# Optimization experiments

Measured on AMD Instinct MI355X. Metric: run time of the kernel, lower is better.

## Reference

```python
import jax, jax.numpy as jnp
import numpy as np

B, D, H, E, TOP_K = 16384, 256, 1024, 8, 2


def setup_inputs() -> dict:
    key = jax.random.key(0)
    ks = jax.random.split(key, 12)
    s = 0.02
    return {
        "t": jax.random.uniform(ks[0], (B,), dtype=jnp.float32),
        "x": jax.random.normal(ks[1], (B, D), dtype=jnp.float32),
        # router: Linear(D+1,H) -> SiLU -> Linear(H,E)
        "Rw1": jax.random.normal(ks[2], (D + 1, H), dtype=jnp.float32) * s,
        "Rb1": jnp.zeros((H,), dtype=jnp.float32),
        "Rw2": jax.random.normal(ks[3], (H, E), dtype=jnp.float32) * s,
        "Rb2": jnp.zeros((E,), dtype=jnp.float32),
        # stacked expert MLPs: (D+1)->H->H->D for each of E experts
        "Ew1": jax.random.normal(ks[4], (E, D + 1, H), dtype=jnp.float32) * s,
        "Eb1": jnp.zeros((E, H), dtype=jnp.float32),
        "Ew2": jax.random.normal(ks[5], (E, H, H), dtype=jnp.float32) * s,
        "Eb2": jnp.zeros((E, H), dtype=jnp.float32),
        "Ew3": jax.random.normal(ks[6], (E, H, D), dtype=jnp.float32) * s,
        "Eb3": jnp.zeros((E, D), dtype=jnp.float32),
    }


def reference(t, x, Rw1, Rb1, Rw2, Rb2, Ew1, Eb1, Ew2, Eb2, Ew3, Eb3):
    t_vec = t.reshape(-1, 1)                      # (B,1)
    xt = jnp.concatenate([x, t_vec], axis=-1)     # (B,D+1)

    # router logits
    h = jax.nn.silu(xt @ Rw1 + Rb1)
    logits = h @ Rw2 + Rb2                        # (B,E)

    # top-k sparse gating (top_k < num_experts)
    topk_vals, topk_idx = jax.lax.top_k(logits, TOP_K)
    mask = jnp.zeros_like(logits).at[jnp.arange(logits.shape[0])[:, None], topk_idx].set(1.0)
    masked_logits = jnp.where(mask == 0, -jnp.inf, logits)
    alpha = jax.nn.softmax(masked_logits, axis=-1)  # (B,E)

    # dense all-expert MLPs (faithful to the original stack+einsum)
    h1 = jax.nn.silu(jnp.einsum('bi,eih->beh', xt, Ew1) + Eb1)   # (B,E,H)
    h2 = jax.nn.silu(jnp.einsum('beh,ehg->beg', h1, Ew2) + Eb2)  # (B,E,H)
    expert_out = jnp.einsum('beh,ehd->bed', h2, Ew3) + Eb3       # (B,E,D)

    velocity = jnp.einsum('be,bed->bd', alpha, expert_out)       # (B,D)
    return velocity
```

## Files before the change

### kernel.cpp

```cpp
#include <hip/hip_runtime.h>
#include <cstdint>
#include <cstddef>

#define NB   16384
#define DD   256
#define DIN  257
#define KP1  288
#define HH   1024
#define NE   8
#define GMAX 33792
#define GMT  264

#define CTRL_INTS 272

typedef unsigned short u16;
typedef __bf16 bf16x8 __attribute__((ext_vector_type(8)));
typedef float  f32x4  __attribute__((ext_vector_type(4)));
typedef unsigned short u16x4 __attribute__((ext_vector_type(4)));

__device__ __forceinline__ u16 f2bf(float f) {
  union { float f; unsigned u; } v; v.f = f;
  return (u16)((v.u + 0x7FFFu + ((v.u >> 16) & 1u)) >> 16);
}
__device__ __forceinline__ float bf2f(u16 h) {
  union { unsigned u; float f; } v; v.u = ((unsigned)h) << 16;
  return v.f;
}

#define GLDS16(g, l) __builtin_amdgcn_global_load_lds( \
    (const __attribute__((address_space(1))) void*)(g), \
    (__attribute__((address_space(3))) void*)(l), 16, 0, 0)

__device__ __forceinline__ int swz_u16(int row, int q) {
  return row * 32 + ((q ^ ((row >> 1) & 3)) * 8);
}

__global__ void build_xt3(const float* __restrict__ x, const float* __restrict__ t,
                          u16* __restrict__ xh, u16* __restrict__ xm, u16* __restrict__ xl) {
  long i = (long)blockIdx.x * 256 + threadIdx.x;
  int b = (int)(i / 72), qd = (int)(i % 72);
  f32x4 v;
  if (qd < 64)       v = *(const f32x4*)&x[(long)b * DD + qd * 4];
  else if (qd == 64) v = (f32x4){t[b], 0.f, 0.f, 0.f};
  else               v = (f32x4){0.f, 0.f, 0.f, 0.f};
  u16x4 h, m, l;
  #pragma unroll
  for (int j = 0; j < 4; ++j) {
    u16 hi = f2bf(v[j]);  float r1 = v[j] - bf2f(hi);
    u16 mi = f2bf(r1);    float r2 = r1 - bf2f(mi);
    h[j] = hi; m[j] = mi; l[j] = f2bf(r2);
  }
  long o = (long)b * KP1 + qd * 4;
  *(u16x4*)&xh[o] = h;  *(u16x4*)&xm[o] = m;  *(u16x4*)&xl[o] = l;
}

__global__ void transpose_w(const float* __restrict__ W, u16* __restrict__ Wh,
                            u16* __restrict__ Wm, u16* __restrict__ Wl,
                            int Kdim, int Ndim, int Kpad, long sW, long sWt) {
  __shared__ float tile[32][33];
  int e = blockIdx.z;
  int k0 = blockIdx.x * 32, n0 = blockIdx.y * 32;
  int tx = threadIdx.x, ty = threadIdx.y;
  const float* Wb = W + (long)e * sW;
  #pragma unroll
  for (int i = 0; i < 4; ++i) {
    int k = k0 + ty + i * 8;
    tile[ty + i * 8][tx] = (k < Kdim) ? Wb[(long)k * Ndim + (n0 + tx)] : 0.f;
  }
  __syncthreads();
  #pragma unroll
  for (int i = 0; i < 4; ++i) {
    int n = n0 + ty + i * 8;
    float v = tile[tx][ty + i * 8];
    long o = (long)e * sWt + (long)n * Kpad + k0 + tx;
    u16 hi = f2bf(v);
    Wh[o] = hi;
    if (Wm) {
      float r1 = v - bf2f(hi);
      u16 mi = f2bf(r1);
      Wm[o] = mi;
      Wl[o] = f2bf(r1 - bf2f(mi));
    }
  }
}

__global__ __launch_bounds__(256, 2)
void router_gemm_emul3(const u16* __restrict__ Ah, const u16* __restrict__ Am, const u16* __restrict__ Al,
                       const u16* __restrict__ Bh, const u16* __restrict__ Bm, const u16* __restrict__ Bl,
                       const float* __restrict__ bias, const float* __restrict__ Rw2,
                       float* __restrict__ pbuf) {
  __shared__ __align__(16) u16 S[6][128 * 32];
  int tid = threadIdx.x;
  int bid = blockIdx.x;
  int xcd = bid & 7, j = bid >> 3;
  int mt = (j >> 3) * 8 + xcd, nt = j & 7;
  int m0 = mt * 128, n0 = nt * 128;
  const u16* Ap[3] = {Ah, Am, Al};
  const u16* Bp[3] = {Bh, Bm, Bl};
  const u16 *ag[3][2], *bg[3][2];
  u16 *la[3][2], *lb[3][2];
  #pragma unroll
  for (int r = 0; r < 2; ++r) {
    int i = r * 256 + tid;
    int row = i >> 2;
    int qa = (i & 3) ^ ((row >> 1) & 3);
    int kq = qa * 8;
    #pragma unroll
    for (int p = 0; p < 3; ++p) {
      ag[p][r] = Ap[p] + (long)(m0 + row) * KP1 + kq;
      bg[p][r] = Bp[p] + (long)(n0 + row) * KP1 + kq;
      la[p][r] = &S[p][i * 8];
      lb[p][r] = &S[3 + p][i * 8];
    }
  }
  int lane = tid & 63, wv = tid >> 6;
  int wm = wv >> 1, wn = wv & 1;
  int q = lane >> 4, c = lane & 15;
  int offA[4], offB[4];
  #pragma unroll
  for (int t4 = 0; t4 < 4; ++t4) {
    offA[t4] = swz_u16(wm * 64 + t4 * 16 + c, q);
    offB[t4] = swz_u16(wn * 64 + t4 * 16 + c, q);
  }
  f32x4 acc[4][4];
  #pragma unroll
  for (int mi = 0; mi < 4; ++mi)
    #pragma unroll
    for (int ni = 0; ni < 4; ++ni) acc[mi][ni] = (f32x4){0.f, 0.f, 0.f, 0.f};

  for (int k0 = 0; k0 < KP1; k0 += 32) {
    __syncthreads();
    #pragma unroll
    for (int r = 0; r < 2; ++r)
      #pragma unroll
      for (int p = 0; p < 3; ++p) {
        GLDS16(ag[p][r] + k0, la[p][r]);
        GLDS16(bg[p][r] + k0, lb[p][r]);
      }
    __syncthreads();
    bf16x8 av[3][4], bv[3][4];
    #pragma unroll
    for (int mi = 0; mi < 4; ++mi)
      #pragma unroll
      for (int p = 0; p < 3; ++p) av[p][mi] = *(const bf16x8*)&S[p][offA[mi]];
    #pragma unroll
    for (int ni = 0; ni < 4; ++ni)
      #pragma unroll
      for (int p = 0; p < 3; ++p) bv[p][ni] = *(const bf16x8*)&S[3 + p][offB[ni]];
    #pragma unroll
    for (int mi = 0; mi < 4; ++mi)
      #pragma unroll
      for (int ni = 0; ni < 4; ++ni) {
        acc[mi][ni] = __builtin_amdgcn_mfma_f32_16x16x32_bf16(av[0][mi], bv[0][ni], acc[mi][ni], 0, 0, 0);
        acc[mi][ni] = __builtin_amdgcn_mfma_f32_16x16x32_bf16(av[0][mi], bv[1][ni], acc[mi][ni], 0, 0, 0);
        acc[mi][ni] = __builtin_amdgcn_mfma_f32_16x16x32_bf16(av[1][mi], bv[0][ni], acc[mi][ni], 0, 0, 0);
        acc[mi][ni] = __builtin_amdgcn_mfma_f32_16x16x32_bf16(av[0][mi], bv[2][ni], acc[mi][ni], 0, 0, 0);
        acc[mi][ni] = __builtin_amdgcn_mfma_f32_16x16x32_bf16(av[2][mi], bv[0][ni], acc[mi][ni], 0, 0, 0);
      }
  }
  float rw2f[4][8];
  #pragma unroll
  for (int ni = 0; ni < 4; ++ni) {
    const float* p = Rw2 + (long)(n0 + wn * 64 + ni * 16 + c) * NE;
    f32x4 a = *(const f32x4*)p, b2 = *(const f32x4*)(p + 4);
    #pragma unroll
    for (int j2 = 0; j2 < 4; ++j2) { rw2f[ni][j2] = a[j2]; rw2f[ni][4 + j2] = b2[j2]; }
  }
  float bi[4];
  #pragma unroll
  for (int ni = 0; ni < 4; ++ni) bi[ni] = bias[n0 + wn * 64 + ni * 16 + c];
  #pragma unroll
  for (int mi = 0; mi < 4; ++mi)
    #pragma unroll
    for (int r = 0; r < 4; ++r) {
      int token = m0 + wm * 64 + mi * 16 + q * 4 + r;
      float part[8] = {0.f, 0.f, 0.f, 0.f, 0.f, 0.f, 0.f, 0.f};
      #pragma unroll
      for (int ni = 0; ni < 4; ++ni) {
        float v = acc[mi][ni][r] + bi[ni];
        v = v / (1.f + expf(-v));
        #pragma unroll
        for (int e = 0; e < 8; ++e) part[e] += v * rw2f[ni][e];
      }
      #pragma unroll
      for (int m = 1; m < 16; m <<= 1)
        #pragma unroll
        for (int e = 0; e < 8; ++e) part[e] += __shfl_xor(part[e], m, 64);
      if (c == 0) {
        float* dst = pbuf + ((long)(nt * 2 + wn) * NB + token) * 8;
        *(f32x4*)dst       = (f32x4){part[0], part[1], part[2], part[3]};
        *(f32x4*)(dst + 4) = (f32x4){part[4], part[5], part[6], part[7]};
      }
    }
}

__global__ void reduce_topk(const float* __restrict__ pbuf, const float* __restrict__ Rb2,
                            int* __restrict__ tk_idx, float* __restrict__ tk_alpha,
                            int* __restrict__ ctrl) {
  __shared__ int lh[NE];
  int tid = threadIdx.x;
  if (tid < NE) lh[tid] = 0;
  __syncthreads();
  int token = blockIdx.x * 256 + tid;
  float v[8];
  #pragma unroll
  for (int e = 0; e < 8; ++e) v[e] = Rb2[e];
  #pragma unroll
  for (int p = 0; p < 16; ++p) {
    const float* src = pbuf + ((long)p * NB + token) * 8;
    f32x4 a = *(const f32x4*)src, b = *(const f32x4*)(src + 4);
    #pragma unroll
    for (int j = 0; j < 4; ++j) { v[j] += a[j]; v[4 + j] += b[j]; }
  }
  int i0 = 0;
  #pragma unroll
  for (int e = 1; e < NE; ++e) if (v[e] > v[i0]) i0 = e;
  int i1 = -1;
  #pragma unroll
  for (int e = 0; e < NE; ++e) { if (e == i0) continue; if (i1 < 0 || v[e] > v[i1]) i1 = e; }
  float d  = v[i1] - v[i0];
  float e1 = expf(d);
  float a0 = 1.f / (1.f + e1);
  float a1 = e1 / (1.f + e1);
  tk_idx[token * 2]     = i0;  tk_idx[token * 2 + 1]   = i1;
  tk_alpha[token * 2]   = a0;  tk_alpha[token * 2 + 1] = a1;
  atomicAdd(&lh[i0], 1);  atomicAdd(&lh[i1], 1);
  __syncthreads();
  if (tid < NE) atomicAdd(&ctrl[tid * 16], lh[tid]);
}

__global__ void compute_offsets(int* __restrict__ ctrl) {
  if (threadIdx.x == 0 && blockIdx.x == 0) {
    int total = 0;
    for (int e = 0; e < NE; ++e) {
      ctrl[256 + e] = total;
      total += (ctrl[e * 16] + 127) & ~127;
    }
    ctrl[256 + NE] = total;
  }
}

__global__ void build_rowmap(const int* __restrict__ tk_idx, int* __restrict__ ctrl,
                             int* __restrict__ grow, int* __restrict__ tok2slot) {
  __shared__ int lh[NE];
  __shared__ int gb[NE];
  int tid = threadIdx.x;
  if (tid < NE) lh[tid] = 0;
  __syncthreads();
  int token = blockIdx.x * 256 + tid;
  int e0 = tk_idx[token * 2], e1 = tk_idx[token * 2 + 1];
  int l0 = atomicAdd(&lh[e0], 1);
  int l1 = atomicAdd(&lh[e1], 1);
  __syncthreads();
  if (tid < NE) gb[tid] = atomicAdd(&ctrl[128 + tid * 16], lh[tid]);
  __syncthreads();
  int g0 = ctrl[256 + e0] + gb[e0] + l0;
  int g1 = ctrl[256 + e1] + gb[e1] + l1;
  grow[g0] = token;  grow[g1] = token;
  tok2slot[token * 2] = g0;  tok2slot[token * 2 + 1] = g1;
}

template<int NKT, int NT, bool GATHER, bool SILU, bool OUTF32>
__global__ __launch_bounds__(256, 2)
void gemm_grouped(const u16* __restrict__ A, int lda,
                  const u16* __restrict__ Wt, long wstride, int ldw,
                  const float* __restrict__ bias, int bstride,
                  u16* __restrict__ C, int ldc,
                  float* __restrict__ Out, int ldo,
                  const int* __restrict__ offp,
                  const int* __restrict__ grow,
                  int K) {
  int bid = blockIdx.x;
  int xcd = bid & 7, j = bid >> 3;
  int mt = (j / NT) * 8 + xcd, nt = j % NT;
  int m0 = mt * 128, n0 = nt * 128;
  if (m0 >= offp[NE]) return;
  int e = 0;
  while (m0 >= offp[e + 1]) ++e;
  __shared__ __align__(16) u16 As[NKT][128 * 32];
  __shared__ __align__(16) u16 Bs[NKT][128 * 32];
  int tid = threadIdx.x;
  const u16 *ag[NKT][2], *bg[NKT][2];
  u16 *la[NKT][2], *lb[NKT][2];
  #pragma unroll
  for (int s = 0; s < NKT; ++s)
    #pragma unroll
    for (int r = 0; r < 2; ++r) {
      int i = r * 256 + tid;
      int row = i >> 2;
      int qa = (i & 3) ^ ((row >> 1) & 3);
      int kq = qa * 8 + s * 32;
      long arow = m0 + row;
      if (GATHER) arow = grow[arow];
      ag[s][r] = A + arow * lda + kq;
      bg[s][r] = Wt + (long)e * wstride + (long)(n0 + row) * ldw + kq;
      la[s][r] = &As[s][i * 8];
      lb[s][r] = &Bs[s][i * 8];
    }
  int lane = tid & 63, wv = tid >> 6;
  int wm = wv >> 1, wn = wv & 1;
  int q = lane >> 4, c = lane & 15;
  int offA[4], offB[4];
  #pragma unroll
  for (int t4 = 0; t4 < 4; ++t4) {
    offA[t4] = swz_u16(wm * 64 + t4 * 16 + c, q);
    offB[t4] = swz_u16(wn * 64 + t4 * 16 + c, q);
  }
  f32x4 acc[4][4];
  #pragma unroll
  for (int mi = 0; mi < 4; ++mi)
    #pragma unroll
    for (int ni = 0; ni < 4; ++ni) acc[mi][ni] = (f32x4){0.f, 0.f, 0.f, 0.f};

  for (int k0 = 0; k0 < K; k0 += 32 * NKT) {
    __syncthreads();
    #pragma unroll
    for (int s = 0; s < NKT; ++s)
      #pragma unroll
      for (int r = 0; r < 2; ++r) {
        GLDS16(ag[s][r] + k0, la[s][r]);
        GLDS16(bg[s][r] + k0, lb[s][r]);
      }
    __syncthreads();
    #pragma unroll
    for (int s = 0; s < NKT; ++s) {
      bf16x8 av[4], bv[4];
      #pragma unroll
      for (int mi = 0; mi < 4; ++mi)
        av[mi] = *(const bf16x8*)&As[s][offA[mi]];
      #pragma unroll
      for (int ni = 0; ni < 4; ++ni)
        bv[ni] = *(const bf16x8*)&Bs[s][offB[ni]];
      #pragma unroll
      for (int mi = 0; mi < 4; ++mi)
        #pragma unroll
        for (int ni = 0; ni < 4; ++ni)
          acc[mi][ni] = __builtin_amdgcn_mfma_f32_16x16x32_bf16(av[mi], bv[ni], acc[mi][ni], 0, 0, 0);
    }
  }
  #pragma unroll
  for (int mi = 0; mi < 4; ++mi)
    #pragma unroll
    for (int r = 0; r < 4; ++r) {
      int row = wm * 64 + mi * 16 + q * 4 + r;
      #pragma unroll
      for (int ni = 0; ni < 4; ++ni) {
        int col = n0 + wn * 64 + ni * 16 + c;
        float v = acc[mi][ni][r] + bias[e * bstride + col];
        if constexpr (SILU) v = v / (1.f + __expf(-v));
        if constexpr (OUTF32) {
          Out[(long)(m0 + row) * ldo + col] = v;
        } else {
          C[(long)(m0 + row) * ldc + col] = f2bf(v);
        }
      }
    }
}

__global__ void combine_out(const float* __restrict__ eo, const int* __restrict__ tok2slot,
                            const float* __restrict__ tk_alpha, float* __restrict__ out) {
  int i = blockIdx.x * 256 + threadIdx.x;
  int token = i >> 6, c4 = (i & 63) * 4;
  long s0 = tok2slot[token * 2], s1 = tok2slot[token * 2 + 1];
  float a0 = tk_alpha[token * 2], a1 = tk_alpha[token * 2 + 1];
  f32x4 v0 = *(const f32x4*)&eo[s0 * DD + c4];
  f32x4 v1 = *(const f32x4*)&eo[s1 * DD + c4];
  f32x4 r;
  #pragma unroll
  for (int j = 0; j < 4; ++j) r[j] = a0 * v0[j] + a1 * v1[j];
  *(f32x4*)&out[(long)token * DD + c4] = r;
}

extern "C" void kernel_launch(void* const* d_in, const int* in_sizes, int n_in,
                              void* d_out, int out_size, void* d_ws, size_t ws_size,
                              hipStream_t stream) {
  const float* t   = (const float*)d_in[0];
  const float* x   = (const float*)d_in[1];
  const float* Rw1 = (const float*)d_in[2];
  const float* Rb1 = (const float*)d_in[3];
  const float* Rw2 = (const float*)d_in[4];
  const float* Rb2 = (const float*)d_in[5];
  const float* Eb1 = (const float*)d_in[7];
  const float* Ew1 = (const float*)d_in[6];
  const float* Ew2 = (const float*)d_in[8];
  const float* Eb2 = (const float*)d_in[9];
  const float* Ew3 = (const float*)d_in[10];
  const float* Eb3 = (const float*)d_in[11];
  float* out = (float*)d_out;

  char* w = (char*)d_ws;
  size_t off = 0;
  auto alloc = [&](size_t bytes) { char* p = w + off; off = (off + bytes + 255) & ~(size_t)255; return p; };
  int*   ctrl     = (int*)  alloc(CTRL_INTS * 4);
  int*   grow     = (int*)  alloc((size_t)GMAX * 4);
  size_t zero_end = off;
  int*   tok2slot = (int*)  alloc((size_t)NB * 2 * 4);
  int*   tk_idx   = (int*)  alloc((size_t)NB * 2 * 4);
  float* tk_alpha = (float*)alloc((size_t)NB * 2 * 4);
  float* pbuf     = (float*)alloc((size_t)16 * NB * 8 * 4);
  u16* xh  = (u16*)alloc((size_t)NB * KP1 * 2);
  u16* xm  = (u16*)alloc((size_t)NB * KP1 * 2);
  u16* xl  = (u16*)alloc((size_t)NB * KP1 * 2);
  u16* R1h = (u16*)alloc((size_t)HH * KP1 * 2);
  u16* R1m = (u16*)alloc((size_t)HH * KP1 * 2);
  u16* R1l = (u16*)alloc((size_t)HH * KP1 * 2);
  u16* E1t = (u16*)alloc((size_t)NE * HH * KP1 * 2);
  u16* E2t = (u16*)alloc((size_t)NE * HH * HH * 2);
  u16* E3t = (u16*)alloc((size_t)NE * DD * HH * 2);
  u16* H1  = (u16*)alloc((size_t)GMAX * HH * 2);
  u16* H2  = (u16*)alloc((size_t)GMAX * HH * 2);
  float* eo = (float*)H1;

  hipMemsetAsync(d_ws, 0, zero_end, stream);

  build_xt3<<<(NB * 72) / 256, 256, 0, stream>>>(x, t, xh, xm, xl);
  dim3 tb(32, 8);
  transpose_w<<<dim3(KP1 / 32, HH / 32, 1),  tb, 0, stream>>>(Rw1, R1h, R1m, R1l, DIN, HH, KP1, 0, 0);
  transpose_w<<<dim3(KP1 / 32, HH / 32, NE), tb, 0, stream>>>(Ew1, E1t, nullptr, nullptr, DIN, HH, KP1, (long)DIN * HH, (long)HH * KP1);
  transpose_w<<<dim3(HH / 32, HH / 32, NE),  tb, 0, stream>>>(Ew2, E2t, nullptr, nullptr, HH, HH, HH, (long)HH * HH, (long)HH * HH);
  transpose_w<<<dim3(HH / 32, DD / 32, NE),  tb, 0, stream>>>(Ew3, E3t, nullptr, nullptr, HH, DD, HH, (long)HH * DD, (long)DD * HH);

  router_gemm_emul3<<<(NB / 128) * 8, 256, 0, stream>>>(xh, xm, xl, R1h, R1m, R1l, Rb1, Rw2, pbuf);
  reduce_topk<<<NB / 256, 256, 0, stream>>>(pbuf, Rb2, tk_idx, tk_alpha, ctrl);
  compute_offsets<<<1, 64, 0, stream>>>(ctrl);
  build_rowmap<<<NB / 256, 256, 0, stream>>>(tk_idx, ctrl, grow, tok2slot);

  const int* offp = ctrl + 256;
  gemm_grouped<3, 8, true, true, false><<<GMT * 8, 256, 0, stream>>>(
      xh, KP1, E1t, (long)HH * KP1, KP1, Eb1, HH, H1, HH, nullptr, 0, offp, grow, KP1);
  gemm_grouped<2, 8, false, true, false><<<GMT * 8, 256, 0, stream>>>(
      H1, HH, E2t, (long)HH * HH, HH, Eb2, HH, H2, HH, nullptr, 0, offp, nullptr, HH);
  gemm_grouped<2, 2, false, false, true><<<GMT * 2, 256, 0, stream>>>(
      H2, HH, E3t, (long)DD * HH, HH, Eb3, DD, nullptr, 0, eo, DD, offp, nullptr, HH);
  combine_out<<<(NB * DD / 4) / 256, 256, 0, stream>>>(eo, tok2slot, tk_alpha, out);
}
```

Baseline: 407.7 us.

## Merge weight transposes into one launch, fold offsets into topk, raise GEMM occupancy

Merges the four weight-transpose launches into one kernel that picks its work from a flat block index. The prefix-offset computation moves into the last block of reduce_topk, found through an atomic counter, so a separate single-thread launch goes away. The grouped GEMM launch bounds rise from 2 to 3 or 4 waves per SIMD to allow more occupancy. The higher bound may cap registers and cause spills. The last-block pattern depends on ctrl[270] being zeroed by the memset, which it is because it lies in the cleared region.

```diff
diff --git a/kernel.cpp b/kernel.cpp
--- a/kernel.cpp
+++ b/kernel.cpp
@@ -54,12 +54,29 @@
   *(u16x4*)&xh[o] = h;  *(u16x4*)&xm[o] = m;  *(u16x4*)&xl[o] = l;
 }
 
-__global__ void transpose_w(const float* __restrict__ W, u16* __restrict__ Wh,
-                            u16* __restrict__ Wm, u16* __restrict__ Wl,
-                            int Kdim, int Ndim, int Kpad, long sW, long sWt) {
+__global__ void transpose_all(const float* __restrict__ Rw1, const float* __restrict__ Ew1,
+                              const float* __restrict__ Ew2, const float* __restrict__ Ew3,
+                              u16* __restrict__ R1h, u16* __restrict__ R1m, u16* __restrict__ R1l,
+                              u16* __restrict__ E1t, u16* __restrict__ E2t, u16* __restrict__ E3t) {
   __shared__ float tile[32][33];
-  int e = blockIdx.z;
-  int k0 = blockIdx.x * 32, n0 = blockIdx.y * 32;
+  int bid = blockIdx.x;
+  const float* W; u16 *Wh, *Wm = nullptr, *Wl = nullptr;
+  int Kdim, Ndim, Kpad, e = 0, kt, nt;
+  long sW = 0, sWt = 0;
+  if (bid < 288) {
+    kt = bid % 9; nt = bid / 9;
+    W = Rw1; Wh = R1h; Wm = R1m; Wl = R1l; Kdim = DIN; Ndim = HH; Kpad = KP1;
+  } else if (bid < 2592) {
+    int b = bid - 288; e = b / 288; b %= 288; kt = b % 9; nt = b / 9;
+    W = Ew1; Wh = E1t; Kdim = DIN; Ndim = HH; Kpad = KP1; sW = (long)DIN * HH; sWt = (long)HH * KP1;
+  } else if (bid < 10784) {
+    int b = bid - 2592; e = b / 1024; b %= 1024; kt = b % 32; nt = b / 32;
+    W = Ew2; Wh = E2t; Kdim = HH; Ndim = HH; Kpad = HH; sW = (long)HH * HH; sWt = (long)HH * HH;
+  } else {
+    int b = bid - 10784; e = b / 256; b %= 256; kt = b % 32; nt = b / 32;
+    W = Ew3; Wh = E3t; Kdim = HH; Ndim = DD; Kpad = HH; sW = (long)HH * DD; sWt = (long)DD * HH;
+  }
+  int k0 = kt * 32, n0 = nt * 32;
   int tx = threadIdx.x, ty = threadIdx.y;
   const float* Wb = W + (long)e * sW;
   #pragma unroll
@@ -227,16 +244,18 @@
   atomicAdd(&lh[i0], 1);  atomicAdd(&lh[i1], 1);
   __syncthreads();
   if (tid < NE) atomicAdd(&ctrl[tid * 16], lh[tid]);
-}
-
-__global__ void compute_offsets(int* __restrict__ ctrl) {
-  if (threadIdx.x == 0 && blockIdx.x == 0) {
-    int total = 0;
-    for (int e = 0; e < NE; ++e) {
-      ctrl[256 + e] = total;
-      total += (ctrl[e * 16] + 127) & ~127;
-    }
-    ctrl[256 + NE] = total;
+  __syncthreads();
+  if (tid == 0) {
+    __threadfence();
+    int done = atomicAdd(&ctrl[270], 1);
+    if (done == gridDim.x - 1) {
+      int total = 0;
+      for (int e = 0; e < NE; ++e) {
+        ctrl[256 + e] = total;
+        total += (atomicAdd(&ctrl[e * 16], 0) + 127) & ~127;
+      }
+      ctrl[256 + NE] = total;
+    }
   }
 }
 
@@ -260,8 +279,8 @@
   tok2slot[token * 2] = g0;  tok2slot[token * 2 + 1] = g1;
 }
 
-template<int NKT, int NT, bool GATHER, bool SILU, bool OUTF32>
-__global__ __launch_bounds__(256, 2)
+template<int NKT, int NT, int MINW, bool GATHER, bool SILU, bool OUTF32>
+__global__ __launch_bounds__(256, MINW)
 void gemm_grouped(const u16* __restrict__ A, int lda,
                   const u16* __restrict__ Wt, long wstride, int ldw,
                   const float* __restrict__ bias, int bstride,
@@ -380,8 +399,8 @@
   const float* Rb1 = (const float*)d_in[3];
   const float* Rw2 = (const float*)d_in[4];
   const float* Rb2 = (const float*)d_in[5];
+  const float* Ew1 = (const float*)d_in[6];
   const float* Eb1 = (const float*)d_in[7];
-  const float* Ew1 = (const float*)d_in[6];
   const float* Ew2 = (const float*)d_in[8];
   const float* Eb2 = (const float*)d_in[9];
   const float* Ew3 = (const float*)d_in[10];
@@ -414,23 +433,19 @@
   hipMemsetAsync(d_ws, 0, zero_end, stream);
 
   build_xt3<<<(NB * 72) / 256, 256, 0, stream>>>(x, t, xh, xm, xl);
-  dim3 tb(32, 8);
-  transpose_w<<<dim3(KP1 / 32, HH / 32, 1),  tb, 0, stream>>>(Rw1, R1h, R1m, R1l, DIN, HH, KP1, 0, 0);
-  transpose_w<<<dim3(KP1 / 32, HH / 32, NE), tb, 0, stream>>>(Ew1, E1t, nullptr, nullptr, DIN, HH, KP1, (long)DIN * HH, (long)HH * KP1);
-  transpose_w<<<dim3(HH / 32, HH / 32, NE),  tb, 0, stream>>>(Ew2, E2t, nullptr, nullptr, HH, HH, HH, (long)HH * HH, (long)HH * HH);
-  transpose_w<<<dim3(HH / 32, DD / 32, NE),  tb, 0, stream>>>(Ew3, E3t, nullptr, nullptr, HH, DD, HH, (long)HH * DD, (long)DD * HH);
+  transpose_all<<<12832, dim3(32, 8), 0, stream>>>(Rw1, Ew1, Ew2, Ew3,
+                                                   R1h, R1m, R1l, E1t, E2t, E3t);
 
   router_gemm_emul3<<<(NB / 128) * 8, 256, 0, stream>>>(xh, xm, xl, R1h, R1m, R1l, Rb1, Rw2, pbuf);
   reduce_topk<<<NB / 256, 256, 0, stream>>>(pbuf, Rb2, tk_idx, tk_alpha, ctrl);
-  compute_offsets<<<1, 64, 0, stream>>>(ctrl);
   build_rowmap<<<NB / 256, 256, 0, stream>>>(tk_idx, ctrl, grow, tok2slot);
 
   const int* offp = ctrl + 256;
-  gemm_grouped<3, 8, true, true, false><<<GMT * 8, 256, 0, stream>>>(
+  gemm_grouped<3, 8, 3, true, true, false><<<GMT * 8, 256, 0, stream>>>(
       xh, KP1, E1t, (long)HH * KP1, KP1, Eb1, HH, H1, HH, nullptr, 0, offp, grow, KP1);
-  gemm_grouped<2, 8, false, true, false><<<GMT * 8, 256, 0, stream>>>(
+  gemm_grouped<2, 8, 4, false, true, false><<<GMT * 8, 256, 0, stream>>>(
       H1, HH, E2t, (long)HH * HH, HH, Eb2, HH, H2, HH, nullptr, 0, offp, nullptr, HH);
-  gemm_grouped<2, 2, false, false, true><<<GMT * 2, 256, 0, stream>>>(
+  gemm_grouped<2, 2, 4, false, false, true><<<GMT * 2, 256, 0, stream>>>(
       H2, HH, E3t, (long)DD * HH, HH, Eb3, DD, nullptr, 0, eo, DD, offp, nullptr, HH);
   combine_out<<<(NB * DD / 4) / 256, 256, 0, stream>>>(eo, tok2slot, tk_alpha, out);
 }
```

Result: faster. 398.6 us (-2.2%).
